# Kernel optimization log

Hardware: AMD Instinct MI355X
Metric: run time of the kernel (lower is better)

Reference implementation:

```python
import jax, jax.numpy as jnp
import numpy as np

B, S, D = 64, 14, 2048   # batch, enc_image_size, encoder_dim
A, H, E = 512, 512, 512  # attention_dim, lstm_size, embedding_size
V, L = 10000, 20         # vocab_size, max caption length (T = L-1 decode steps)


def setup_inputs() -> dict:
    key = jax.random.key(0)
    ks = jax.random.split(key, 24)
    p = lambda k, shape: jax.random.normal(k, shape, jnp.float32) * 0.02
    features = jax.random.normal(ks[0], (B, S, S, D), jnp.float32)
    captions = jax.random.randint(ks[1], (B, L), 0, V)
    # sorted descending lengths in [2, L], max forced to L so T_dec = L-1
    lengths = jnp.sort(jax.random.randint(ks[2], (B,), 2, L + 1))[::-1]
    lengths = lengths.at[0].set(L)
    return {
        'features': features, 'captions': captions, 'lengths': lengths,
        'emb': p(ks[3], (V, E)),
        'W_ih': p(ks[4], (4 * H, D + E)), 'b_ih': p(ks[5], (4 * H,)),
        'W_hh': p(ks[6], (4 * H, H)), 'b_hh': p(ks[7], (4 * H,)),
        'h_fc_w': p(ks[8], (H, D)), 'h_fc_b': p(ks[9], (H,)),
        'c_fc_w': p(ks[10], (H, D)), 'c_fc_b': p(ks[11], (H,)),
        'f_beta_w': p(ks[12], (D, H)), 'f_beta_b': p(ks[13], (D,)),
        'cls_w': p(ks[14], (V, H)), 'cls_b': p(ks[15], (V,)),
        'enc_w': p(ks[16], (A, D)), 'enc_b': p(ks[17], (A,)),
        'dec_w': p(ks[18], (A, H)), 'dec_b': p(ks[19], (A,)),
        'att_w': p(ks[20], (1, A)), 'att_b': p(ks[21], (1,)),
    }


def reference(features, captions, lengths, emb, W_ih, b_ih, W_hh, b_hh,
              h_fc_w, h_fc_b, c_fc_w, c_fc_b, f_beta_w, f_beta_b,
              cls_w, cls_b, enc_w, enc_b, dec_w, dec_b, att_w, att_b):
    feats = features.reshape(features.shape[0], -1, features.shape[-1])  # (B,P,D)
    emb_seq = emb[captions]                                              # (B,L,E)
    mean_f = feats.mean(axis=1)
    h = mean_f @ h_fc_w.T + h_fc_b
    c = mean_f @ c_fc_w.T + c_fc_b
    dec_len = lengths - 1
    T = captions.shape[1] - 1
    # attention encoder projection is time-invariant: hoist out of the loop
    att1 = jnp.einsum('bpd,ad->bpa', feats, enc_w) + enc_b               # (B,P,A)

    def step(carry, xs):
        h, c = carry
        x_emb, t = xs
        att2 = h @ dec_w.T + dec_b                                       # (B,A)
        e = jnp.einsum('bpa,a->bp', jax.nn.relu(att1 + att2[:, None, :]), att_w[0]) + att_b[0]
        alpha = jax.nn.softmax(e, axis=1)                                # (B,P)
        awe = jnp.einsum('bp,bpd->bd', alpha, feats)
        gate = jax.nn.sigmoid(h @ f_beta_w.T + f_beta_b)
        awe = gate * awe
        x = jnp.concatenate([x_emb, awe], axis=1)                        # (B,E+D)
        gates = x @ W_ih.T + b_ih + h @ W_hh.T + b_hh                    # torch gate order i,f,g,o
        i, f, g, o = jnp.split(gates, 4, axis=1)
        c2 = jax.nn.sigmoid(f) * c + jax.nn.sigmoid(i) * jnp.tanh(g)
        h2 = jax.nn.sigmoid(o) * jnp.tanh(c2)
        y = h2 @ cls_w.T + cls_b                                         # dropout = eval identity
        active = (t < dec_len)[:, None]
        return (h2, c2), (jnp.where(active, y, 0.0), jnp.where(active, alpha, 0.0))

    xs = (jnp.swapaxes(emb_seq[:, :T], 0, 1), jnp.arange(T))
    (_, _), (y_pred, alphas) = jax.lax.scan(step, (h, c), xs)
    return jnp.swapaxes(y_pred, 0, 1), jnp.swapaxes(alphas, 0, 1)
```

## Files before the change

kernel.cpp:

```cpp
#include <hip/hip_runtime.h>
#include <math.h>

typedef __attribute__((ext_vector_type(8))) short bf16x8;
typedef __attribute__((ext_vector_type(8))) unsigned short u16x8;
typedef __attribute__((ext_vector_type(4))) float f32x4;

#define NB 64
#define NP 196
#define ND 2048
#define NA 512
#define NH 512
#define NE 512
#define NV 10000
#define NT 19
#define NROW (NB*NP)
#define NVP 10112
#define MROW 1280
#define NHP 4608

__device__ __forceinline__ unsigned short f2bu(float f){
    unsigned int u; __builtin_memcpy(&u, &f, 4);
    u = (u + 0x7FFFu + ((u >> 16) & 1u)) >> 16;
    return (unsigned short)u;
}
__device__ __forceinline__ float b2f(unsigned short s){
    unsigned int u = ((unsigned int)s) << 16;
    float f; __builtin_memcpy(&f, &u, 4); return f;
}
__device__ __forceinline__ float sigm(float x){ return 1.f/(1.f + __expf(-x)); }

__device__ __forceinline__ void gll16(const void* g, void* l){
    __builtin_amdgcn_global_load_lds(
        (const __attribute__((address_space(1))) void*)g,
        (__attribute__((address_space(3))) void*)l, 16, 0, 0);
}


__global__ void k_prep(const float4* __restrict__ enc_w, const float4* __restrict__ dec_w,
                       const float4* __restrict__ f_beta_w, const float4* __restrict__ W_ih,
                       const float4* __restrict__ W_hh, const float4* __restrict__ h_fc_w,
                       const float4* __restrict__ c_fc_w, const float4* __restrict__ cls_w,
                       ushort4* __restrict__ encwb, ushort4* __restrict__ whp,
                       ushort4* __restrict__ wgates, ushort4* __restrict__ wembb,
                       ushort4* __restrict__ whc, ushort4* __restrict__ clswb,
                       ushort4* __restrict__ hsb_pad){
    const int n0 = NA*ND/4;
    const int n1 = NHP*512/4;
    const int n2 = 2048*2048/4;
    const int n3 = 2048*512/4;
    const int n4 = 1024*2048/4;
    const int n5 = NVP*NH/4;
    const int n6 = 64*512/4;
    const int total = n0+n1+n2+n3+n4+n5+n6;
    int stride = gridDim.x*blockDim.x;
    for (int i = blockIdx.x*blockDim.x + threadIdx.x; i < total; i += stride){
        int idx = i;
        float4 v; ushort4 o;
        if (idx < n0){
            v = enc_w[idx];
            o.x = f2bu(v.x); o.y = f2bu(v.y); o.z = f2bu(v.z); o.w = f2bu(v.w);
            encwb[idx] = o; continue;
        }
        idx -= n0;
        if (idx < n1){
            if (idx < 512*512/4) v = dec_w[idx];
            else if (idx < 2560*512/4) v = f_beta_w[idx - 512*512/4];
            else v = W_hh[idx - 2560*512/4];
            o.x = f2bu(v.x); o.y = f2bu(v.y); o.z = f2bu(v.z); o.w = f2bu(v.w);
            whp[idx] = o; continue;
        }
        idx -= n1;
        if (idx < n2){
            int j = idx >> 9, kk4 = idx & 511;
            v = W_ih[(size_t)j*640 + 128 + kk4];
            o.x = f2bu(v.x); o.y = f2bu(v.y); o.z = f2bu(v.z); o.w = f2bu(v.w);
            wgates[idx] = o; continue;
        }
        idx -= n2;
        if (idx < n3){
            int j = idx >> 7, kk4 = idx & 127;
            v = W_ih[(size_t)j*640 + kk4];
            o.x = f2bu(v.x); o.y = f2bu(v.y); o.z = f2bu(v.z); o.w = f2bu(v.w);
            wembb[idx] = o; continue;
        }
        idx -= n3;
        if (idx < n4){
            v = (idx < 512*2048/4) ? h_fc_w[idx] : c_fc_w[idx - 512*2048/4];
            o.x = f2bu(v.x); o.y = f2bu(v.y); o.z = f2bu(v.z); o.w = f2bu(v.w);
            whc[idx] = o; continue;
        }
        idx -= n4;
        if (idx < n5){
            if (idx < NV*NH/4){
                v = cls_w[idx];
                o.x = f2bu(v.x); o.y = f2bu(v.y); o.z = f2bu(v.z); o.w = f2bu(v.w);
            } else { o.x = 0; o.y = 0; o.z = 0; o.w = 0; }
            clswb[idx] = o; continue;
        }
        idx -= n5;
        o.x = 0; o.y = 0; o.z = 0; o.w = 0;
        hsb_pad[idx] = o;
    }
}

__global__ void k_cm(const float* __restrict__ feats,
                     unsigned short* __restrict__ fbf,
                     unsigned short* __restrict__ meanbf){
    __shared__ float4 msum[256];
    int dc = blockIdx.x;
    int b  = blockIdx.y;
    int tid = threadIdx.x;
    int c4 = tid & 63;
    int rq = tid >> 6;
    int D0 = dc*256;
    float4 acc = {0.f,0.f,0.f,0.f};
    for (int p = rq; p < NP; p += 4){
        float4 v = *(const float4*)(feats + ((size_t)(b*NP + p))*ND + D0 + c4*4);
        acc.x += v.x; acc.y += v.y; acc.z += v.z; acc.w += v.w;
        ushort4 u4;
        u4.x = f2bu(v.x); u4.y = f2bu(v.y); u4.z = f2bu(v.z); u4.w = f2bu(v.w);
        *(ushort4*)(fbf + ((size_t)(b*NP + p))*ND + D0 + c4*4) = u4;
    }
    msum[tid] = acc;
    __syncthreads();
    if (tid < 64){
        float4 s0 = msum[tid], s1 = msum[tid+64], s2 = msum[tid+128], s3 = msum[tid+192];
        float4 tot = { (s0.x+s1.x)+(s2.x+s3.x), (s0.y+s1.y)+(s2.y+s3.y),
                       (s0.z+s1.z)+(s2.z+s3.z), (s0.w+s1.w)+(s2.w+s3.w) };
        ushort4 o;
        o.x = f2bu(tot.x*(1.f/196.f)); o.y = f2bu(tot.y*(1.f/196.f));
        o.z = f2bu(tot.z*(1.f/196.f)); o.w = f2bu(tot.w*(1.f/196.f));
        *(ushort4*)(meanbf + (size_t)b*ND + D0 + tid*4) = o;
    }
}

__global__ void k_embg(const float* __restrict__ emb, const int* __restrict__ captions,
                       unsigned short* __restrict__ embcat){
    int blk = blockIdx.x, tid = threadIdx.x;
    int r = blk*4 + (tid >> 6);
    int cg = tid & 63;
    u16x8 o;
    #pragma unroll
    for (int k = 0; k < 8; k++) o[k] = 0;
    if (r < NT*64){
        int t = r >> 6, b = r & 63;
        int tok = captions[b*20 + t];
        const float* e = emb + (size_t)tok*NE + cg*8;
        float4 v0 = *(const float4*)e;
        float4 v1 = *(const float4*)(e + 4);
        o[0] = f2bu(v0.x); o[1] = f2bu(v0.y); o[2] = f2bu(v0.z); o[3] = f2bu(v0.w);
        o[4] = f2bu(v1.x); o[5] = f2bu(v1.y); o[6] = f2bu(v1.z); o[7] = f2bu(v1.w);
    }
    *(u16x8*)(embcat + (size_t)r*NE + cg*8) = o;
}

__global__ void k_hc0m(const unsigned short* __restrict__ meanbf,
                       const unsigned short* __restrict__ whc,
                       const float* __restrict__ h_fc_b, const float* __restrict__ c_fc_b,
                       unsigned short* __restrict__ hbf, float* __restrict__ cst){
    int tid = threadIdx.x;
    int w = tid >> 6, l = tid & 63;
    int nt = blockIdx.x;
    int row = 16*w + (l & 15);
    int col = nt*16 + (l & 15);
    int kg = (l >> 4) * 8;
    f32x4 acc = {};
    for (int k0 = 0; k0 < ND; k0 += 32){
        bf16x8 af = *(const bf16x8*)(meanbf + (size_t)row*ND + k0 + kg);
        bf16x8 bv = *(const bf16x8*)(whc + (size_t)col*ND + k0 + kg);
        acc = __builtin_amdgcn_mfma_f32_16x16x32_bf16(af, bv, acc, 0, 0, 0);
    }
    int r0 = 16*w + (l >> 4)*4;
    #pragma unroll
    for (int r = 0; r < 4; r++){
        int b = r0 + r;
        if (col < 512) hbf[b*NH + col] = f2bu(acc[r] + h_fc_b[col]);
        else           cst[b*NH + (col - 512)] = acc[r] + c_fc_b[col - 512];
    }
}

template<int K>
__device__ __forceinline__ void gemm128(const unsigned short* __restrict__ A,
                                        const unsigned short* __restrict__ B,
                                        int brow, int bcol, f32x4 acc[4][4]){
    __shared__ unsigned short As[128*32];
    __shared__ unsigned short Bs[128*32];
    int tid = threadIdx.x;
    int w = tid >> 6, l = tid & 63;
    int wr = (w >> 1) * 64, wc = (w & 1) * 64;
    int lr = l & 15, kg = (l >> 4) * 8;
    const unsigned short* ga0 = A + (size_t)(brow + (tid >> 2))*K + (tid & 3)*8;
    const unsigned short* gb0 = B + (size_t)(bcol + (tid >> 2))*K + (tid & 3)*8;
    for (int k0 = 0; k0 < K; k0 += 32){
        __syncthreads();
        gll16(ga0 + k0,                As + w*512);
        gll16(ga0 + (size_t)64*K + k0, As + 2048 + w*512);
        gll16(gb0 + k0,                Bs + w*512);
        gll16(gb0 + (size_t)64*K + k0, Bs + 2048 + w*512);
        __syncthreads();
        bf16x8 af[4], bfr[4];
        #pragma unroll
        for (int mi = 0; mi < 4; mi++)
            af[mi] = *(const bf16x8*)(As + (wr + mi*16 + lr)*32 + kg);
        #pragma unroll
        for (int ni = 0; ni < 4; ni++)
            bfr[ni] = *(const bf16x8*)(Bs + (wc + ni*16 + lr)*32 + kg);
        #pragma unroll
        for (int ni = 0; ni < 4; ni++){
            #pragma unroll
            for (int mi = 0; mi < 4; mi++)
                acc[mi][ni] = __builtin_amdgcn_mfma_f32_16x16x32_bf16(af[mi], bfr[ni], acc[mi][ni], 0, 0, 0);
        }
    }
}

__global__ void k_gemm_att1(const unsigned short* __restrict__ fbf,
                            const unsigned short* __restrict__ encw,
                            const float* __restrict__ enc_b,
                            unsigned short* __restrict__ att1){
    f32x4 acc[4][4] = {};
    int brow = blockIdx.x*128, bcol = blockIdx.y*128;
    gemm128<ND>(fbf, encw, brow, bcol, acc);
    int w = threadIdx.x >> 6, l = threadIdx.x & 63;
    int wr = (w >> 1) * 64, wc = (w & 1) * 64;
    int r0 = brow + wr + (l >> 4)*4;
    int c0 = bcol + wc + (l & 15);
    #pragma unroll
    for (int ni = 0; ni < 4; ni++){
        int col = c0 + ni*16;
        float eb = enc_b[col];
        #pragma unroll
        for (int mi = 0; mi < 4; mi++){
            #pragma unroll
            for (int r = 0; r < 4; r++)
                att1[(size_t)(r0 + mi*16 + r)*NA + col] = f2bu(acc[mi][ni][r] + eb);
        }
    }
}

__global__ void k_gemb(const unsigned short* __restrict__ embcat,
                       const unsigned short* __restrict__ wembb,
                       const float* __restrict__ b_ih, const float* __restrict__ b_hh,
                       float* __restrict__ gemb){
    f32x4 acc[4][4] = {};
    int brow = blockIdx.x*128, bcol = blockIdx.y*128;
    gemm128<NE>(embcat, wembb, brow, bcol, acc);
    int w = threadIdx.x >> 6, l = threadIdx.x & 63;
    int wr = (w >> 1) * 64, wc = (w & 1) * 64;
    int r0 = brow + wr + (l >> 4)*4;
    int c0 = bcol + wc + (l & 15);
    #pragma unroll
    for (int ni = 0; ni < 4; ni++){
        int col = c0 + ni*16;
        float bias = b_ih[col] + b_hh[col];
        #pragma unroll
        for (int mi = 0; mi < 4; mi++){
            #pragma unroll
            for (int r = 0; r < 4; r++)
                gemb[(size_t)(r0 + mi*16 + r)*2048 + col] = acc[mi][ni][r] + bias;
        }
    }
}

__global__ void k_gemm_cls(const unsigned short* __restrict__ hsb,
                           const unsigned short* __restrict__ clsw,
                           const float* __restrict__ cls_b,
                           const int* __restrict__ lengths,
                           float* __restrict__ yout){
    f32x4 acc[4][4] = {};
    int brow = blockIdx.x*128, bcol = blockIdx.y*128;
    gemm128<NH>(hsb, clsw, brow, bcol, acc);
    int w = threadIdx.x >> 6, l = threadIdx.x & 63;
    int wr = (w >> 1) * 64, wc = (w & 1) * 64;
    int r0 = brow + wr + (l >> 4)*4;
    int c0 = bcol + wc + (l & 15);
    #pragma unroll
    for (int ni = 0; ni < 4; ni++){
        int col = c0 + ni*16;
        if (col >= NV) continue;
        float cb = cls_b[col];
        #pragma unroll
        for (int mi = 0; mi < 4; mi++){
            #pragma unroll
            for (int r = 0; r < 4; r++){
                int grow = r0 + mi*16 + r;
                if (grow >= NT*64) continue;
                int t = grow >> 6, bb = grow & 63;
                int active = t < (lengths[bb] - 1);
                yout[((size_t)bb*NT + t)*NV + col] = active ? (acc[mi][ni][r] + cb) : 0.f;
            }
        }
    }
}


__global__ void k_lstm(const float* __restrict__ part, const float* __restrict__ gemb,
                       const float* __restrict__ hp,
                       float* __restrict__ cst, unsigned short* __restrict__ hbf,
                       unsigned short* __restrict__ hsb, int t){
    int idx = blockIdx.x*256 + threadIdx.x;
    int b = idx >> 9, j = idx & 511;
    const float* ge = gemb + ((size_t)(t - 1)*64 + b)*2048;
    const float* hh = hp + (size_t)b*NHP + 2560;
    float gi = ge[j]        + hh[j];
    float gf = ge[512 + j]  + hh[512 + j];
    float gg = ge[1024 + j] + hh[1024 + j];
    float go = ge[1536 + j] + hh[1536 + j];
    #pragma unroll
    for (int s = 0; s < 8; s++){
        const float* pb = part + (size_t)(s*64 + b)*2048;
        gi += pb[j]; gf += pb[512 + j]; gg += pb[1024 + j]; go += pb[1536 + j];
    }
    float c = cst[b*NH + j];
    float c2 = sigm(gf)*c + sigm(gi)*tanhf(gg);
    float h2 = sigm(go)*tanhf(c2);
    cst[b*NH + j] = c2;
    unsigned short u = f2bu(h2);
    hbf[b*NH + j] = u;
    hsb[((size_t)(t - 1)*64 + b)*NH + j] = u;
}

__global__ void k_hall(const unsigned short* __restrict__ hbf,
                       const unsigned short* __restrict__ whp,
                       const float* __restrict__ dec_b, const float* __restrict__ f_beta_b,
                       float* __restrict__ hp){
    int w = threadIdx.x >> 6, l = threadIdx.x & 63;
    int nt = blockIdx.x;
    int row = 16*w + (l & 15);
    int col = nt*16 + (l & 15);
    int kg = (l >> 4) * 8;
    f32x4 acc = {};
    for (int k0 = 0; k0 < NH; k0 += 32){
        bf16x8 af = *(const bf16x8*)(hbf + row*NH + k0 + kg);
        bf16x8 bv = *(const bf16x8*)(whp + (size_t)col*NH + k0 + kg);
        acc = __builtin_amdgcn_mfma_f32_16x16x32_bf16(af, bv, acc, 0, 0, 0);
    }
    int r0 = 16*w + (l >> 4)*4;
    float bias = (col < 512) ? dec_b[col] : ((col < 2560) ? f_beta_b[col - 512] : 0.f);
    #pragma unroll
    for (int r = 0; r < 4; r++)
        hp[(size_t)(r0 + r)*NHP + col] = acc[r] + bias;
}

__global__ void k_eawe(const unsigned short* __restrict__ att1,
                       const float* __restrict__ hp,
                       const unsigned short* __restrict__ fbf,
                       const float* __restrict__ att_w, const float* __restrict__ att_b,
                       const int* __restrict__ lengths,
                       unsigned short* __restrict__ xg, float* __restrict__ alphas, int t){
    __shared__ float at2[NA];
    __shared__ float aw[NA];
    __shared__ float al[NP];
    __shared__ float red[256];
    int dc = blockIdx.x;
    int b  = blockIdx.y;
    int tid = threadIdx.x;
    for (int j = tid; j < NA; j += 256){
        at2[j] = hp[(size_t)b*NHP + j];
        aw[j]  = att_w[j];
    }
    __syncthreads();
    float s = -1e30f;
    if (tid < NP){
        const unsigned short* arow = att1 + ((size_t)(b*NP + tid))*NA;
        float c0 = 0.f, c1 = 0.f, c2 = 0.f, c3 = 0.f;
        for (int a0 = 0; a0 < 512; a0 += 8){
            bf16x8 v = *(const bf16x8*)(arow + a0);
            #pragma unroll
            for (int e = 0; e < 8; e++){
                float x = b2f((unsigned short)v[e]) + at2[a0 + e];
                float m = fmaxf(x, 0.f) * aw[a0 + e];
                if ((e & 3) == 0) c0 += m; else if ((e & 3) == 1) c1 += m;
                else if ((e & 3) == 2) c2 += m; else c3 += m;
            }
        }
        s = att_b[0] + (c0 + c1) + (c2 + c3);
    }
    red[tid] = s; __syncthreads();
    for (int st = 128; st > 0; st >>= 1){ if (tid < st) red[tid] = fmaxf(red[tid], red[tid+st]); __syncthreads(); }
    float m = red[0]; __syncthreads();
    float ev = (tid < NP) ? __expf(s - m) : 0.f;
    red[tid] = ev; __syncthreads();
    for (int st = 128; st > 0; st >>= 1){ if (tid < st) red[tid] += red[tid+st]; __syncthreads(); }
    float inv = 1.f / red[0];
    if (tid < NP) al[tid] = ev * inv;
    __syncthreads();
    if (dc == 0 && tid < NP){
        int active = t < (lengths[b] - 1);
        alphas[((size_t)b*NT + t)*NP + tid] = active ? al[tid] : 0.f;
    }
    int d = dc*1024 + tid*4;
    const unsigned short* fb = fbf + (size_t)(b*NP)*ND + d;
    float a0 = 0.f, a1 = 0.f, a2 = 0.f, a3 = 0.f;
    #pragma unroll 4
    for (int p = 0; p < NP; p++){
        ushort4 v = *(const ushort4*)(fb + (size_t)p*ND);
        float ap = al[p];
        a0 += ap * b2f(v.x); a1 += ap * b2f(v.y);
        a2 += ap * b2f(v.z); a3 += ap * b2f(v.w);
    }
    float4 hb = *(const float4*)(hp + (size_t)b*NHP + 512 + d);
    ushort4 o;
    o.x = f2bu(sigm(hb.x) * a0); o.y = f2bu(sigm(hb.y) * a1);
    o.z = f2bu(sigm(hb.z) * a2); o.w = f2bu(sigm(hb.w) * a3);
    *(ushort4*)(xg + b*2048 + d) = o;
}

__global__ void k_gates(const unsigned short* __restrict__ xg,
                        const unsigned short* __restrict__ wgates,
                        float* __restrict__ part){
    int nt = blockIdx.x;
    int s  = blockIdx.y;
    int w = threadIdx.x >> 6, l = threadIdx.x & 63;
    int row = 16*w + (l & 15);
    int col = nt*16 + (l & 15);
    int kg = (l >> 4) * 8;
    const unsigned short* arow = xg + row*2048 + s*256;
    const unsigned short* brow = wgates + (size_t)col*2048 + s*256;
    f32x4 acc = {};
    for (int k0 = 0; k0 < 256; k0 += 32){
        bf16x8 af = *(const bf16x8*)(arow + k0 + kg);
        bf16x8 bv = *(const bf16x8*)(brow + k0 + kg);
        acc = __builtin_amdgcn_mfma_f32_16x16x32_bf16(af, bv, acc, 0, 0, 0);
    }
    int r0 = 16*w + (l >> 4)*4;
    #pragma unroll
    for (int r = 0; r < 4; r++)
        part[(size_t)(s*64 + r0 + r)*2048 + col] = acc[r];
}

__global__ void k_lstm_fin(const float* __restrict__ part, const float* __restrict__ gemb,
                           const float* __restrict__ hp,
                           const float* __restrict__ cst, unsigned short* __restrict__ hsb){
    int idx = blockIdx.x*256 + threadIdx.x;
    int b = idx >> 9, j = idx & 511;
    const float* ge = gemb + ((size_t)(NT - 1)*64 + b)*2048;
    const float* hh = hp + (size_t)b*NHP + 2560;
    float gi = ge[j]        + hh[j];
    float gf = ge[512 + j]  + hh[512 + j];
    float gg = ge[1024 + j] + hh[1024 + j];
    float go = ge[1536 + j] + hh[1536 + j];
    #pragma unroll
    for (int s = 0; s < 8; s++){
        const float* pb = part + (size_t)(s*64 + b)*2048;
        gi += pb[j]; gf += pb[512 + j]; gg += pb[1024 + j]; go += pb[1536 + j];
    }
    float c = cst[b*NH + j];
    float c2 = sigm(gf)*c + sigm(gi)*tanhf(gg);
    float h2 = sigm(go)*tanhf(c2);
    hsb[((size_t)(NT - 1)*64 + b)*NH + j] = f2bu(h2);
}


extern "C" void kernel_launch(void* const* d_in, const int* in_sizes, int n_in,
                              void* d_out, int out_size, void* d_ws, size_t ws_size,
                              hipStream_t stream){
    const float* features = (const float*)d_in[0];
    const int*   captions = (const int*)d_in[1];
    const int*   lengths  = (const int*)d_in[2];
    const float* emb      = (const float*)d_in[3];
    const float* W_ih     = (const float*)d_in[4];
    const float* b_ih     = (const float*)d_in[5];
    const float* W_hh     = (const float*)d_in[6];
    const float* b_hh     = (const float*)d_in[7];
    const float* h_fc_w   = (const float*)d_in[8];
    const float* h_fc_b   = (const float*)d_in[9];
    const float* c_fc_w   = (const float*)d_in[10];
    const float* c_fc_b   = (const float*)d_in[11];
    const float* f_beta_w = (const float*)d_in[12];
    const float* f_beta_b = (const float*)d_in[13];
    const float* cls_w    = (const float*)d_in[14];
    const float* cls_b    = (const float*)d_in[15];
    const float* enc_w    = (const float*)d_in[16];
    const float* enc_b    = (const float*)d_in[17];
    const float* dec_w    = (const float*)d_in[18];
    const float* dec_b    = (const float*)d_in[19];
    const float* att_w    = (const float*)d_in[20];
    const float* att_b    = (const float*)d_in[21];

    char* w = (char*)d_ws;
    size_t off = 0;
    auto alloc = [&](size_t bytes)->char*{
        char* p = w + off;
        off += (bytes + 255) & ~(size_t)255;
        return p;
    };
    unsigned short* fbf    = (unsigned short*)alloc((size_t)NROW*ND*2);
    unsigned short* att1   = (unsigned short*)alloc((size_t)NROW*NA*2);
    unsigned short* encwb  = (unsigned short*)alloc((size_t)NA*ND*2);
    unsigned short* whp    = (unsigned short*)alloc((size_t)NHP*NH*2);
    unsigned short* wgates = (unsigned short*)alloc((size_t)2048*2048*2);
    unsigned short* wembb  = (unsigned short*)alloc((size_t)2048*NE*2);
    unsigned short* whc    = (unsigned short*)alloc((size_t)1024*ND*2);
    unsigned short* clswb  = (unsigned short*)alloc((size_t)NVP*NH*2);
    unsigned short* embcat = (unsigned short*)alloc((size_t)MROW*NE*2);
    unsigned short* hsb    = (unsigned short*)alloc((size_t)MROW*NH*2);
    unsigned short* hbf    = (unsigned short*)alloc((size_t)64*NH*2);
    unsigned short* xg     = (unsigned short*)alloc((size_t)64*2048*2);
    unsigned short* meanbf = (unsigned short*)alloc((size_t)64*ND*2);
    float* gemb  = (float*)alloc((size_t)MROW*2048*4);
    float* cst   = (float*)alloc((size_t)64*NH*4);
    float* hp    = (float*)alloc((size_t)64*NHP*4);
    float* part  = (float*)alloc((size_t)8*64*2048*4);

    float* yout = (float*)d_out;
    float* alphas_out = yout + (size_t)NB*NT*NV;

    k_cm<<<dim3(8, 64), 256, 0, stream>>>(features, fbf, meanbf);
    k_prep<<<2048, 256, 0, stream>>>((const float4*)enc_w, (const float4*)dec_w,
                                     (const float4*)f_beta_w, (const float4*)W_ih,
                                     (const float4*)W_hh, (const float4*)h_fc_w,
                                     (const float4*)c_fc_w, (const float4*)cls_w,
                                     (ushort4*)encwb, (ushort4*)whp, (ushort4*)wgates,
                                     (ushort4*)wembb, (ushort4*)whc, (ushort4*)clswb,
                                     (ushort4*)(hsb + (size_t)NT*64*NH));
    k_embg<<<320, 256, 0, stream>>>(emb, captions, embcat);
    k_hc0m<<<64, 256, 0, stream>>>(meanbf, whc, h_fc_b, c_fc_b, hbf, cst);
    k_gemm_att1<<<dim3(98, 4), 256, 0, stream>>>(fbf, encwb, enc_b, att1);
    k_gemb<<<dim3(10, 16), 256, 0, stream>>>(embcat, wembb, b_ih, b_hh, gemb);

    for (int t = 0; t < NT; t++){
        if (t > 0)
            k_lstm<<<128, 256, 0, stream>>>(part, gemb, hp, cst, hbf, hsb, t);
        k_hall<<<288, 256, 0, stream>>>(hbf, whp, dec_b, f_beta_b, hp);
        k_eawe<<<dim3(2, 64), 256, 0, stream>>>(att1, hp, fbf, att_w, att_b,
                                                lengths, xg, alphas_out, t);
        k_gates<<<dim3(128, 8), 256, 0, stream>>>(xg, wgates, part);
    }
    k_lstm_fin<<<128, 256, 0, stream>>>(part, gemb, hp, cst, hsb);
    k_gemm_cls<<<dim3(10, 79), 256, 0, stream>>>(hsb, clswb, cls_b, lengths, yout);
}
```

Measured before the change: 1.252 ms.

## Split attention score and weighted-sum into separate kernels with wider parallelism

The fused attention kernel ran only 128 blocks, each recomputing all 196 scores. Scores are now computed once per batch in a new kernel, with four threads per pixel and a shuffle reduction, and written to a small buffer. A second kernel reads them, runs the softmax, and forms the weighted sum over 512 blocks with one output column per thread. This spreads the serial per-timestep work across many more CUs, at the cost of an extra launch per step, scalar 2-byte loads in place of 8-byte vector loads, and each block redoing the softmax.

```diff
diff --git a/kernel.cpp b/kernel.cpp
--- a/kernel.cpp
+++ b/kernel.cpp
@@ -342,46 +342,54 @@
         hp[(size_t)(r0 + r)*NHP + col] = acc[r] + bias;
 }
 
-__global__ void k_eawe(const unsigned short* __restrict__ att1,
-                       const float* __restrict__ hp,
-                       const unsigned short* __restrict__ fbf,
-                       const float* __restrict__ att_w, const float* __restrict__ att_b,
-                       const int* __restrict__ lengths,
-                       unsigned short* __restrict__ xg, float* __restrict__ alphas, int t){
+__global__ void k_e(const unsigned short* __restrict__ att1,
+                    const float* __restrict__ hp,
+                    const float* __restrict__ att_w, const float* __restrict__ att_b,
+                    float* __restrict__ ews){
     __shared__ float at2[NA];
     __shared__ float aw[NA];
+    int b = blockIdx.x >> 2, pc = blockIdx.x & 3;
+    int tid = threadIdx.x;
+    for (int j = tid; j < NA; j += 256){
+        at2[j] = hp[(size_t)b*NHP + j];
+        aw[j]  = att_w[j];
+    }
+    __syncthreads();
+    int pl = tid >> 2, q = tid & 3;
+    if (pl < 49){
+        int p = pc*49 + pl;
+        const unsigned short* arow = att1 + ((size_t)(b*NP + p))*NA + q*128;
+        float s = 0.f;
+        for (int a0 = 0; a0 < 128; a0 += 8){
+            bf16x8 v = *(const bf16x8*)(arow + a0);
+            #pragma unroll
+            for (int e = 0; e < 8; e++){
+                int ai = q*128 + a0 + e;
+                float x = b2f((unsigned short)v[e]) + at2[ai];
+                s += fmaxf(x, 0.f) * aw[ai];
+            }
+        }
+        s += __shfl_xor(s, 1);
+        s += __shfl_xor(s, 2);
+        if (q == 0) ews[b*NP + p] = s + att_b[0];
+    }
+}
+
+__global__ void k_awe(const float* __restrict__ ews, const unsigned short* __restrict__ fbf,
+                      const float* __restrict__ hp, const int* __restrict__ lengths,
+                      unsigned short* __restrict__ xg, float* __restrict__ alphas, int t){
     __shared__ float al[NP];
     __shared__ float red[256];
     int dc = blockIdx.x;
     int b  = blockIdx.y;
     int tid = threadIdx.x;
-    for (int j = tid; j < NA; j += 256){
-        at2[j] = hp[(size_t)b*NHP + j];
-        aw[j]  = att_w[j];
-    }
-    __syncthreads();
-    float s = -1e30f;
-    if (tid < NP){
-        const unsigned short* arow = att1 + ((size_t)(b*NP + tid))*NA;
-        float c0 = 0.f, c1 = 0.f, c2 = 0.f, c3 = 0.f;
-        for (int a0 = 0; a0 < 512; a0 += 8){
-            bf16x8 v = *(const bf16x8*)(arow + a0);
-            #pragma unroll
-            for (int e = 0; e < 8; e++){
-                float x = b2f((unsigned short)v[e]) + at2[a0 + e];
-                float m = fmaxf(x, 0.f) * aw[a0 + e];
-                if ((e & 3) == 0) c0 += m; else if ((e & 3) == 1) c1 += m;
-                else if ((e & 3) == 2) c2 += m; else c3 += m;
-            }
-        }
-        s = att_b[0] + (c0 + c1) + (c2 + c3);
-    }
-    red[tid] = s; __syncthreads();
-    for (int st = 128; st > 0; st >>= 1){ if (tid < st) red[tid] = fmaxf(red[tid], red[tid+st]); __syncthreads(); }
+    float v = (tid < NP) ? ews[b*NP + tid] : -1e30f;
+    red[tid] = v; __syncthreads();
+    for (int s = 128; s > 0; s >>= 1){ if (tid < s) red[tid] = fmaxf(red[tid], red[tid+s]); __syncthreads(); }
     float m = red[0]; __syncthreads();
-    float ev = (tid < NP) ? __expf(s - m) : 0.f;
+    float ev = (tid < NP) ? __expf(v - m) : 0.f;
     red[tid] = ev; __syncthreads();
-    for (int st = 128; st > 0; st >>= 1){ if (tid < st) red[tid] += red[tid+st]; __syncthreads(); }
+    for (int s = 128; s > 0; s >>= 1){ if (tid < s) red[tid] += red[tid+s]; __syncthreads(); }
     float inv = 1.f / red[0];
     if (tid < NP) al[tid] = ev * inv;
     __syncthreads();
@@ -389,21 +397,18 @@
         int active = t < (lengths[b] - 1);
         alphas[((size_t)b*NT + t)*NP + tid] = active ? al[tid] : 0.f;
     }
-    int d = dc*1024 + tid*4;
+    int d = dc*256 + tid;
     const unsigned short* fb = fbf + (size_t)(b*NP)*ND + d;
     float a0 = 0.f, a1 = 0.f, a2 = 0.f, a3 = 0.f;
-    #pragma unroll 4
-    for (int p = 0; p < NP; p++){
-        ushort4 v = *(const ushort4*)(fb + (size_t)p*ND);
-        float ap = al[p];
-        a0 += ap * b2f(v.x); a1 += ap * b2f(v.y);
-        a2 += ap * b2f(v.z); a3 += ap * b2f(v.w);
-    }
-    float4 hb = *(const float4*)(hp + (size_t)b*NHP + 512 + d);
-    ushort4 o;
-    o.x = f2bu(sigm(hb.x) * a0); o.y = f2bu(sigm(hb.y) * a1);
-    o.z = f2bu(sigm(hb.z) * a2); o.w = f2bu(sigm(hb.w) * a3);
-    *(ushort4*)(xg + b*2048 + d) = o;
+    for (int p = 0; p < 196; p += 4){
+        a0 += al[p]     * b2f(fb[(size_t)p*ND]);
+        a1 += al[p + 1] * b2f(fb[(size_t)(p + 1)*ND]);
+        a2 += al[p + 2] * b2f(fb[(size_t)(p + 2)*ND]);
+        a3 += al[p + 3] * b2f(fb[(size_t)(p + 3)*ND]);
+    }
+    float accv = (a0 + a1) + (a2 + a3);
+    float g = sigm(hp[(size_t)b*NHP + 512 + d]);
+    xg[b*2048 + d] = f2bu(g * accv);
 }
 
 __global__ void k_gates(const unsigned short* __restrict__ xg,
@@ -501,6 +506,7 @@
     float* gemb  = (float*)alloc((size_t)MROW*2048*4);
     float* cst   = (float*)alloc((size_t)64*NH*4);
     float* hp    = (float*)alloc((size_t)64*NHP*4);
+    float* ews   = (float*)alloc((size_t)64*NP*4);
     float* part  = (float*)alloc((size_t)8*64*2048*4);
 
     float* yout = (float*)d_out;
@@ -523,8 +529,8 @@
         if (t > 0)
             k_lstm<<<128, 256, 0, stream>>>(part, gemb, hp, cst, hbf, hsb, t);
         k_hall<<<288, 256, 0, stream>>>(hbf, whp, dec_b, f_beta_b, hp);
-        k_eawe<<<dim3(2, 64), 256, 0, stream>>>(att1, hp, fbf, att_w, att_b,
-                                                lengths, xg, alphas_out, t);
+        k_e<<<256, 256, 0, stream>>>(att1, hp, att_w, att_b, ews);
+        k_awe<<<dim3(8, 64), 256, 0, stream>>>(ews, fbf, hp, lengths, xg, alphas_out, t);
         k_gates<<<dim3(128, 8), 256, 0, stream>>>(xg, wgates, part);
     }
     k_lstm_fin<<<128, 256, 0, stream>>>(part, gemb, hp, cst, hsb);
```

After: 1.054 ms. 15.8% less time.
